# Kernel optimization log

Measured on AMD Instinct MI355X. Metric: run time of the kernel, lower is better.

## Reference

```python
import jax, jax.numpy as jnp
import numpy as np

N_USERS = 200000
N_ITEMS = 200000
F_DIM = 128   # raw embedding_dim of u_feature / i_feature
E_DIM = 64    # embed_dim
N_NODES = 100000
K = 24        # threshold for is_user=True (max sampled neighbors)


def setup_inputs() -> dict:
    key = jax.random.key(0)
    ks = jax.random.split(key, 16)
    s = 0.05
    return {
        "nodes": jax.random.randint(ks[0], (N_NODES,), 0, N_USERS),
        "n_feature": jax.random.normal(ks[1], (N_NODES, E_DIM), jnp.float32),
        "neigh_idx": jax.random.randint(ks[2], (N_NODES, K), 0, N_ITEMS),
        "u_weight": jax.random.normal(ks[3], (N_USERS, F_DIM), jnp.float32) * s,
        "i_weight": jax.random.normal(ks[4], (N_ITEMS, F_DIM), jnp.float32) * s,
        "uW": jax.random.normal(ks[5], (F_DIM, E_DIM), jnp.float32) * s,
        "ub": jax.random.normal(ks[6], (E_DIM,), jnp.float32) * s,
        "iW": jax.random.normal(ks[7], (F_DIM, E_DIM), jnp.float32) * s,
        "ib": jax.random.normal(ks[8], (E_DIM,), jnp.float32) * s,
        "aW1": jax.random.normal(ks[9], (2 * E_DIM, E_DIM), jnp.float32) * s,
        "ab1": jax.random.normal(ks[10], (E_DIM,), jnp.float32) * s,
        "aW2": jax.random.normal(ks[11], (E_DIM, E_DIM), jnp.float32) * s,
        "ab2": jax.random.normal(ks[12], (E_DIM,), jnp.float32) * s,
        "aW3": jax.random.normal(ks[13], (E_DIM, 1), jnp.float32) * s,
        "ab3": jax.random.normal(ks[14], (1,), jnp.float32) * s,
    }


def reference(nodes, n_feature, neigh_idx, u_weight, i_weight,
              uW, ub, iW, ib, aW1, ab1, aW2, ab2, aW3, ab3):
    # u_layer applied to gathered user rows (L0Dense in eval mode ~ dense linear)
    nodes_fea = u_weight[nodes] @ uW + ub                       # [N, d]

    # Project the item table once, then gather neighbors (same math, less traffic
    # than gathering raw features per neighbor): i_layer(ifeature.weight[neighs])
    i_proj = i_weight @ iW + ib                                 # [n_items, d]
    neighs = i_proj[neigh_idx]                                  # [N, K, d]

    # query = mean(node_feature + n_feature[i], dim=0) over a [1,d] tensor == the vector itself
    q = nodes_fea + n_feature                                   # [N, d]

    # attention MLP over concat(neighbor, query) -> softmax over K neighbors
    x = jnp.concatenate(
        [neighs, jnp.broadcast_to(q[:, None, :], neighs.shape)], axis=-1)  # [N, K, 2d]
    h = jax.nn.relu(x @ aW1 + ab1)                              # [N, K, d]
    h = jax.nn.relu(h @ aW2 + ab2)                              # [N, K, d]
    scores = (h @ aW3 + ab3)[..., 0]                            # [N, K]
    att_w = jax.nn.softmax(scores, axis=-1)                     # [N, K]

    # attention-weighted aggregation: neighs_feature.T @ att_w per node
    emb = jnp.einsum('nk,nkd->nd', att_w, neighs)               # [N, d]

    # scatter into the full embed_matrix [num_embeddings, d]
    embed_matrix = jnp.zeros((u_weight.shape[0], nodes_fea.shape[1]),
                             nodes_fea.dtype).at[nodes].set(emb)
    return nodes_fea, embed_matrix
```

## Files before the change

### kernel.cpp

```cpp
#include <hip/hip_runtime.h>
#include <hip/hip_bf16.h>

#define N_NODES 100000
#define N_USERS 200000
#define N_ITEMS 200000
#define KNEI 24
#define E 64
#define F 128

typedef __attribute__((ext_vector_type(8))) short bf16x8;
typedef __attribute__((ext_vector_type(4))) float f32x4;


__device__ inline float bf2f(short s) {
    unsigned u = ((unsigned)(unsigned short)s) << 16;
    return __uint_as_float(u);
}
__device__ inline short f2bf(float f) {
    __hip_bfloat16 h = __float2bfloat16(f);
    return *reinterpret_cast<short*>(&h);
}
__device__ inline float rdlane_f(float v, int l) {
    return __uint_as_float(__builtin_amdgcn_readlane(__float_as_uint(v), l));
}
__device__ inline bf16x8 pack8(float4 a, float4 b) {
    bf16x8 r;
    r[0] = f2bf(a.x); r[1] = f2bf(a.y); r[2] = f2bf(a.z); r[3] = f2bf(a.w);
    r[4] = f2bf(b.x); r[5] = f2bf(b.y); r[6] = f2bf(b.z); r[7] = f2bf(b.w);
    return r;
}

__global__ __launch_bounds__(256) void k_fuse(const float* __restrict__ iW,
                                              const float* __restrict__ aW1,
                                              const float* __restrict__ ib,
                                              const float* __restrict__ ab1,
                                              float* __restrict__ Wp,
                                              float* __restrict__ bp) {
    int g = blockIdx.x * 256 + threadIdx.x;
    int f = g >> 6, c = g & 63;
    float s = 0.f;
    for (int j = 0; j < 64; j++) s = fmaf(iW[f * 64 + j], aW1[j * 64 + c], s);
    Wp[g] = s;
    if (g < 64) {
        float b = ab1[g];
        for (int j = 0; j < 64; j++) b = fmaf(ib[j], aW1[j * 64 + g], b);
        bp[g] = b;
    }
}


__global__ __launch_bounds__(256, 2) void k_item(const float* __restrict__ iwt,
                                                 const float* __restrict__ iW,
                                                 const float* __restrict__ ib,
                                                 const float* __restrict__ Wp,
                                                 const float* __restrict__ bp,
                                                 __hip_bfloat16* __restrict__ iproj,
                                                 __hip_bfloat16* __restrict__ iatt) {
    const int wave = threadIdx.x >> 6, lane = threadIdx.x & 63;
    const int lo = lane & 15, hi = lane >> 4;

    bf16x8 B1[4][4], B2[4][4];
    #pragma unroll
    for (int s = 0; s < 4; s++) {
        #pragma unroll
        for (int u = 0; u < 4; u++) {
            bf16x8 b1, b2;
            #pragma unroll
            for (int e = 0; e < 8; e++) {
                int k = 32 * s + 8 * hi + e;
                b1[e] = f2bf(iW[k * 64 + 16 * u + lo]);
                b2[e] = f2bf(Wp[k * 64 + 16 * u + lo]);
            }
            B1[s][u] = b1; B2[s][u] = b2;
        }
    }
    float bi[4], ba[4];
    #pragma unroll
    for (int u = 0; u < 4; u++) { bi[u] = ib[16 * u + lo]; ba[u] = bp[16 * u + lo]; }

    const int wid = blockIdx.x * 4 + wave;
    for (int t = wid; t < N_ITEMS / 16; t += 512 * 4) {
        int r0 = t * 16;
        const float4* Ap = reinterpret_cast<const float4*>(iwt + (size_t)(r0 + lo) * F);
        bf16x8 A[4];
        #pragma unroll
        for (int s = 0; s < 4; s++)
            A[s] = pack8(Ap[8 * s + 2 * hi], Ap[8 * s + 2 * hi + 1]);
        f32x4 acc1[4], acc2[4];
        #pragma unroll
        for (int u = 0; u < 4; u++) {
            acc1[u] = (f32x4){0.f, 0.f, 0.f, 0.f};
            acc2[u] = (f32x4){0.f, 0.f, 0.f, 0.f};
        }
        #pragma unroll
        for (int s = 0; s < 4; s++) {
            #pragma unroll
            for (int u = 0; u < 4; u++) {
                acc1[u] = __builtin_amdgcn_mfma_f32_16x16x32_bf16(A[s], B1[s][u], acc1[u], 0, 0, 0);
                acc2[u] = __builtin_amdgcn_mfma_f32_16x16x32_bf16(A[s], B2[s][u], acc2[u], 0, 0, 0);
            }
        }
        #pragma unroll
        for (int u = 0; u < 4; u++) {
            #pragma unroll
            for (int reg = 0; reg < 4; reg++) {
                size_t off = (size_t)(r0 + 4 * hi + reg) * E + 16 * u + lo;
                iproj[off] = __float2bfloat16(acc1[u][reg] + bi[u]);
                iatt[off]  = __float2bfloat16(acc2[u][reg] + ba[u]);
            }
        }
    }
}

__global__ __launch_bounds__(256, 2) void k_node1(const int* __restrict__ nodes,
                                                  const float* __restrict__ uwt,
                                                  const float* __restrict__ uW,
                                                  const float* __restrict__ ub,
                                                  float* __restrict__ out_nf,
                                                  int* __restrict__ winner) {
    const int wave = threadIdx.x >> 6, lane = threadIdx.x & 63;
    const int lo = lane & 15, hi = lane >> 4;

    bf16x8 B[4][4];
    #pragma unroll
    for (int s = 0; s < 4; s++) {
        #pragma unroll
        for (int u = 0; u < 4; u++) {
            bf16x8 b;
            #pragma unroll
            for (int e = 0; e < 8; e++) {
                int k = 32 * s + 8 * hi + e;
                b[e] = f2bf(uW[k * 64 + 16 * u + lo]);
            }
            B[s][u] = b;
        }
    }
    float bu[4];
    #pragma unroll
    for (int u = 0; u < 4; u++) bu[u] = ub[16 * u + lo];

    const int wid = blockIdx.x * 4 + wave;
    for (int t = wid; t < N_NODES / 16; t += 256 * 4) {
        int r0 = t * 16;
        int n = r0 + lo;
        int un = nodes[n];
        if (hi == 0) atomicMax(&winner[un], n);
        const float4* Ap = reinterpret_cast<const float4*>(uwt + (size_t)un * F);
        bf16x8 A[4];
        #pragma unroll
        for (int s = 0; s < 4; s++)
            A[s] = pack8(Ap[8 * s + 2 * hi], Ap[8 * s + 2 * hi + 1]);
        f32x4 acc[4];
        #pragma unroll
        for (int u = 0; u < 4; u++) acc[u] = (f32x4){0.f, 0.f, 0.f, 0.f};
        #pragma unroll
        for (int s = 0; s < 4; s++) {
            #pragma unroll
            for (int u = 0; u < 4; u++)
                acc[u] = __builtin_amdgcn_mfma_f32_16x16x32_bf16(A[s], B[s][u], acc[u], 0, 0, 0);
        }
        #pragma unroll
        for (int u = 0; u < 4; u++) {
            #pragma unroll
            for (int reg = 0; reg < 4; reg++)
                out_nf[(size_t)(r0 + 4 * hi + reg) * E + 16 * u + lo] = acc[u][reg] + bu[u];
        }
    }
}

__global__ __launch_bounds__(256, 2) void k_node2(const float* __restrict__ out_nf,
                                                  const float* __restrict__ nfeat,
                                                  const float* __restrict__ aW1,
                                                  __hip_bfloat16* __restrict__ qatt) {
    const int wave = threadIdx.x >> 6, lane = threadIdx.x & 63;
    const int lo = lane & 15, hi = lane >> 4;

    bf16x8 B[2][4];
    #pragma unroll
    for (int s = 0; s < 2; s++) {
        #pragma unroll
        for (int u = 0; u < 4; u++) {
            bf16x8 b;
            #pragma unroll
            for (int e = 0; e < 8; e++) {
                int k = 32 * s + 8 * hi + e;
                b[e] = f2bf(aW1[(size_t)(E + k) * 64 + 16 * u + lo]);
            }
            B[s][u] = b;
        }
    }

    const int wid = blockIdx.x * 4 + wave;
    for (int t = wid; t < N_NODES / 16; t += 256 * 4) {
        int r0 = t * 16;
        const float4* Op = reinterpret_cast<const float4*>(out_nf + (size_t)(r0 + lo) * E);
        const float4* Np = reinterpret_cast<const float4*>(nfeat + (size_t)(r0 + lo) * E);
        bf16x8 A[2];
        #pragma unroll
        for (int s = 0; s < 2; s++) {
            float4 o0 = Op[8 * s + 2 * hi], o1 = Op[8 * s + 2 * hi + 1];
            float4 n0 = Np[8 * s + 2 * hi], n1 = Np[8 * s + 2 * hi + 1];
            float4 q0 = make_float4(o0.x + n0.x, o0.y + n0.y, o0.z + n0.z, o0.w + n0.w);
            float4 q1 = make_float4(o1.x + n1.x, o1.y + n1.y, o1.z + n1.z, o1.w + n1.w);
            A[s] = pack8(q0, q1);
        }
        f32x4 acc[4];
        #pragma unroll
        for (int u = 0; u < 4; u++) acc[u] = (f32x4){0.f, 0.f, 0.f, 0.f};
        #pragma unroll
        for (int s = 0; s < 2; s++) {
            #pragma unroll
            for (int u = 0; u < 4; u++)
                acc[u] = __builtin_amdgcn_mfma_f32_16x16x32_bf16(A[s], B[s][u], acc[u], 0, 0, 0);
        }
        #pragma unroll
        for (int u = 0; u < 4; u++) {
            #pragma unroll
            for (int reg = 0; reg < 4; reg++)
                qatt[(size_t)(r0 + 4 * hi + reg) * E + 16 * u + lo] =
                    __float2bfloat16(acc[u][reg]);
        }
    }
}

__global__ __launch_bounds__(256) void k_att(const int* __restrict__ nodes,
                                             const int* __restrict__ nidx,
                                             const __hip_bfloat16* __restrict__ iproj,
                                             const __hip_bfloat16* __restrict__ iatt,
                                             const __hip_bfloat16* __restrict__ qatt,
                                             const float* __restrict__ aW2,
                                             const float* __restrict__ ab2,
                                             const float* __restrict__ aW3,
                                             const int* __restrict__ winner,
                                             float* __restrict__ outE) {
    __shared__ float s_scores[4][192];
    const int wave = threadIdx.x >> 6, lane = threadIdx.x & 63;
    const int lo = lane & 15, hi = lane >> 4;
    const int n0 = (blockIdx.x * 4 + wave) * 8;

    bf16x8 B[2][4];
    #pragma unroll
    for (int s = 0; s < 2; s++) {
        #pragma unroll
        for (int u = 0; u < 4; u++) {
            bf16x8 b;
            #pragma unroll
            for (int e = 0; e < 8; e++) {
                int kk = 32 * s + 8 * hi + e;
                b[e] = f2bf(aW2[(size_t)kk * E + 16 * u + lo]);
            }
            B[s][u] = b;
        }
    }
    float b2c[4], w3c[4];
    #pragma unroll
    for (int u = 0; u < 4; u++) { b2c[u] = ab2[16 * u + lo]; w3c[u] = aW3[16 * u + lo]; }

    int idxs[12], nls[12];
    #pragma unroll
    for (int t = 0; t < 12; t++) {
        int r = t * 16 + lo;
        int nl = r / 24;
        nls[t] = nl;
        idxs[t] = nidx[(size_t)(n0 + nl) * KNEI + (r - nl * 24)];
    }

    #pragma unroll
    for (int t = 0; t < 12; t++) {
        const bf16x8* iarow = reinterpret_cast<const bf16x8*>(iatt + (size_t)idxs[t] * E);
        const bf16x8* qrow  = reinterpret_cast<const bf16x8*>(qatt + (size_t)(n0 + nls[t]) * E);
        f32x4 acc[4];
        #pragma unroll
        for (int u = 0; u < 4; u++) acc[u] = (f32x4){0.f, 0.f, 0.f, 0.f};
        #pragma unroll
        for (int s = 0; s < 2; s++) {
            bf16x8 ia = iarow[4 * s + hi];
            bf16x8 qa = qrow[4 * s + hi];
            bf16x8 a;
            #pragma unroll
            for (int e = 0; e < 8; e++) {
                float v = bf2f(ia[e]) + bf2f(qa[e]);
                a[e] = f2bf(fmaxf(v, 0.f));
            }
            #pragma unroll
            for (int u = 0; u < 4; u++)
                acc[u] = __builtin_amdgcn_mfma_f32_16x16x32_bf16(a, B[s][u], acc[u], 0, 0, 0);
        }
        f32x4 sum;
        #pragma unroll
        for (int reg = 0; reg < 4; reg++) {
            float v = 0.f;
            #pragma unroll
            for (int u = 0; u < 4; u++)
                v += fmaxf(acc[u][reg] + b2c[u], 0.f) * w3c[u];
            sum[reg] = v;
        }
        #pragma unroll
        for (int m = 1; m < 16; m <<= 1) {
            #pragma unroll
            for (int reg = 0; reg < 4; reg++)
                sum[reg] += __shfl_xor(sum[reg], m);
        }
        if (lo == 0)
            *reinterpret_cast<f32x4*>(&s_scores[wave][t * 16 + hi * 4]) = sum;
    }
    __syncthreads();

    #pragma unroll 1
    for (int nd = 0; nd < 8; nd++) {
        int n = n0 + nd;
        int k5 = lane & 31;
        bool kv = k5 < KNEI;
        float sc = kv ? s_scores[wave][nd * KNEI + k5] : -1e30f;
        float mx = sc;
        #pragma unroll
        for (int m = 1; m < 32; m <<= 1) mx = fmaxf(mx, __shfl_xor(mx, m));
        float e = kv ? __expf(sc - mx) : 0.f;
        float ssum = e;
        #pragma unroll
        for (int m = 1; m < 32; m <<= 1) ssum += __shfl_xor(ssum, m);
        float w = e / ssum;
        int idxv = kv ? nidx[(size_t)n * KNEI + k5] : 0;

        float emb = 0.f;
        const short* ip = reinterpret_cast<const short*>(iproj);
        #pragma unroll
        for (int k = 0; k < KNEI; k++) {
            int sidx = __builtin_amdgcn_readlane(idxv, k);
            float wk = rdlane_f(w, k);
            emb = fmaf(wk, bf2f(ip[(size_t)sidx * E + lane]), emb);
        }
        int un = nodes[n];
        if (winner[un] == n) outE[(size_t)un * E + lane] = emb;
    }
}

extern "C" void kernel_launch(void* const* d_in, const int* in_sizes, int n_in,
                              void* d_out, int out_size, void* d_ws, size_t ws_size,
                              hipStream_t stream) {
    const int*   nodes = (const int*)d_in[0];
    const float* nfeat = (const float*)d_in[1];
    const int*   nidx  = (const int*)d_in[2];
    const float* uwt   = (const float*)d_in[3];
    const float* iwt   = (const float*)d_in[4];
    const float* uW    = (const float*)d_in[5];
    const float* ub    = (const float*)d_in[6];
    const float* iW    = (const float*)d_in[7];
    const float* ib    = (const float*)d_in[8];
    const float* aW1   = (const float*)d_in[9];
    const float* ab1   = (const float*)d_in[10];
    const float* aW2   = (const float*)d_in[11];
    const float* ab2   = (const float*)d_in[12];
    const float* aW3   = (const float*)d_in[13];

    float* out_nf  = (float*)d_out;
    float* out_emb = out_nf + (size_t)N_NODES * E;

    char* ws = (char*)d_ws;
    __hip_bfloat16* iproj = (__hip_bfloat16*)(ws);
    __hip_bfloat16* iatt  = (__hip_bfloat16*)(ws + 25600000);
    __hip_bfloat16* qatt  = (__hip_bfloat16*)(ws + 51200000);
    int*            winner = (int*)(ws + 64000000);
    float*          Wp     = (float*)(ws + 64800000);
    float*          bp     = (float*)(ws + 64832768);

    hipMemsetAsync(winner, 0xFF, (size_t)N_USERS * sizeof(int), stream);
    hipMemsetAsync(out_emb, 0, (size_t)N_USERS * E * sizeof(float), stream);

    k_fuse<<<32, 256, 0, stream>>>(iW, aW1, ib, ab1, Wp, bp);
    k_item<<<512, 256, 0, stream>>>(iwt, iW, ib, Wp, bp, iproj, iatt);
    k_node1<<<256, 256, 0, stream>>>(nodes, uwt, uW, ub, out_nf, winner);
    k_node2<<<256, 256, 0, stream>>>(out_nf, nfeat, aW1, qatt);
    k_att<<<N_NODES / 32, 256, 0, stream>>>(nodes, nidx, iproj, iatt, qatt,
                                            aW2, ab2, aW3, winner, out_emb);
}
```

Measured before the change: 236.8 us.

## Precompute aW2 fragment image and rework attention aggregation to process two nodes per wave

Moves the per-wave bf16 conversion and scattered loading of aW2, ab2 and aW3 into the setup kernel, which writes a lane-ordered fragment image that k_att loads with coalesced 16-byte reads. The ab2 bias is folded into the MFMA accumulator initialisation. The aggregation loop now handles two nodes per wave at once, each half-wave reading 4-byte bf16 pairs of iproj rows, with neighbor index and weight pairs staged in LDS instead of readlane. Outputs are stored as float2. This trades extra LDS traffic and a small amount of setup work for fewer redundant weight loads and wider gathers.

After: 208.1 us. 12.1% less time.

```diff
diff --git a/kernel.cpp b/kernel.cpp
--- a/kernel.cpp
+++ b/kernel.cpp
@@ -20,9 +20,6 @@
     __hip_bfloat16 h = __float2bfloat16(f);
     return *reinterpret_cast<short*>(&h);
 }
-__device__ inline float rdlane_f(float v, int l) {
-    return __uint_as_float(__builtin_amdgcn_readlane(__float_as_uint(v), l));
-}
 __device__ inline bf16x8 pack8(float4 a, float4 b) {
     bf16x8 r;
     r[0] = f2bf(a.x); r[1] = f2bf(a.y); r[2] = f2bf(a.z); r[3] = f2bf(a.w);
@@ -34,17 +31,41 @@
                                               const float* __restrict__ aW1,
                                               const float* __restrict__ ib,
                                               const float* __restrict__ ab1,
+                                              const float* __restrict__ aW2,
+                                              const float* __restrict__ ab2,
+                                              const float* __restrict__ aW3,
                                               float* __restrict__ Wp,
-                                              float* __restrict__ bp) {
+                                              float* __restrict__ bp,
+                                              bf16x8* __restrict__ B2img,
+                                              float* __restrict__ bw) {
     int g = blockIdx.x * 256 + threadIdx.x;
-    int f = g >> 6, c = g & 63;
-    float s = 0.f;
-    for (int j = 0; j < 64; j++) s = fmaf(iW[f * 64 + j], aW1[j * 64 + c], s);
-    Wp[g] = s;
-    if (g < 64) {
-        float b = ab1[g];
-        for (int j = 0; j < 64; j++) b = fmaf(ib[j], aW1[j * 64 + g], b);
-        bp[g] = b;
+    if (g < 8192) {
+        int f = g >> 6, c = g & 63;
+        float s = 0.f;
+        for (int j = 0; j < 64; j++) s = fmaf(iW[f * 64 + j], aW1[j * 64 + c], s);
+        Wp[g] = s;
+        if (g < 64) {
+            float b = ab1[g];
+            for (int j = 0; j < 64; j++) b = fmaf(ib[j], aW1[j * 64 + g], b);
+            bp[g] = b;
+        }
+    } else if (g < 8192 + 512) {
+        int h = g - 8192;
+        int f = h >> 6, l = h & 63;
+        int s = f >> 2, u = f & 3;
+        int lo = l & 15, hi = l >> 4;
+        bf16x8 b;
+        #pragma unroll
+        for (int e = 0; e < 8; e++)
+            b[e] = f2bf(aW2[(size_t)(32 * s + 8 * hi + e) * 64 + 16 * u + lo]);
+        B2img[h] = b;
+        if (f == 0) {
+            #pragma unroll
+            for (int uu = 0; uu < 4; uu++) {
+                bw[l * 8 + uu]     = ab2[16 * uu + lo];
+                bw[l * 8 + 4 + uu] = aW3[16 * uu + lo];
+            }
+        }
     }
 }
 
@@ -228,33 +249,21 @@
                                              const __hip_bfloat16* __restrict__ iproj,
                                              const __hip_bfloat16* __restrict__ iatt,
                                              const __hip_bfloat16* __restrict__ qatt,
-                                             const float* __restrict__ aW2,
-                                             const float* __restrict__ ab2,
-                                             const float* __restrict__ aW3,
+                                             const bf16x8* __restrict__ B2img,
+                                             const float* __restrict__ bw,
                                              const int* __restrict__ winner,
                                              float* __restrict__ outE) {
     __shared__ float s_scores[4][192];
+    __shared__ int2  s_iw[4][192];
     const int wave = threadIdx.x >> 6, lane = threadIdx.x & 63;
     const int lo = lane & 15, hi = lane >> 4;
     const int n0 = (blockIdx.x * 4 + wave) * 8;
 
-    bf16x8 B[2][4];
-    #pragma unroll
-    for (int s = 0; s < 2; s++) {
-        #pragma unroll
-        for (int u = 0; u < 4; u++) {
-            bf16x8 b;
-            #pragma unroll
-            for (int e = 0; e < 8; e++) {
-                int kk = 32 * s + 8 * hi + e;
-                b[e] = f2bf(aW2[(size_t)kk * E + 16 * u + lo]);
-            }
-            B[s][u] = b;
-        }
-    }
-    float b2c[4], w3c[4];
-    #pragma unroll
-    for (int u = 0; u < 4; u++) { b2c[u] = ab2[16 * u + lo]; w3c[u] = aW3[16 * u + lo]; }
+    bf16x8 Bf[8];
+    #pragma unroll
+    for (int f = 0; f < 8; f++) Bf[f] = B2img[f * 64 + lane];
+    f32x4 bb = *reinterpret_cast<const f32x4*>(bw + lane * 8);
+    f32x4 wv = *reinterpret_cast<const f32x4*>(bw + lane * 8 + 4);
 
     int idxs[12], nls[12];
     #pragma unroll
@@ -263,6 +272,7 @@
         int nl = r / 24;
         nls[t] = nl;
         idxs[t] = nidx[(size_t)(n0 + nl) * KNEI + (r - nl * 24)];
+        s_iw[wave][r].x = idxs[t];
     }
 
     #pragma unroll
@@ -271,7 +281,8 @@
         const bf16x8* qrow  = reinterpret_cast<const bf16x8*>(qatt + (size_t)(n0 + nls[t]) * E);
         f32x4 acc[4];
         #pragma unroll
-        for (int u = 0; u < 4; u++) acc[u] = (f32x4){0.f, 0.f, 0.f, 0.f};
+        for (int u = 0; u < 4; u++)
+            acc[u] = (f32x4){bb[u], bb[u], bb[u], bb[u]};
         #pragma unroll
         for (int s = 0; s < 2; s++) {
             bf16x8 ia = iarow[4 * s + hi];
@@ -284,7 +295,7 @@
             }
             #pragma unroll
             for (int u = 0; u < 4; u++)
-                acc[u] = __builtin_amdgcn_mfma_f32_16x16x32_bf16(a, B[s][u], acc[u], 0, 0, 0);
+                acc[u] = __builtin_amdgcn_mfma_f32_16x16x32_bf16(a, Bf[s * 4 + u], acc[u], 0, 0, 0);
         }
         f32x4 sum;
         #pragma unroll
@@ -292,7 +303,7 @@
             float v = 0.f;
             #pragma unroll
             for (int u = 0; u < 4; u++)
-                v += fmaxf(acc[u][reg] + b2c[u], 0.f) * w3c[u];
+                v = fmaf(fmaxf(acc[u][reg], 0.f), wv[u], v);
             sum[reg] = v;
         }
         #pragma unroll
@@ -306,32 +317,37 @@
     }
     __syncthreads();
 
-    #pragma unroll 1
-    for (int nd = 0; nd < 8; nd++) {
+    const int half = lane >> 5, j = lane & 31;
+    for (int p = 0; p < 4; p++) {
+        int nd = 2 * p + half;
         int n = n0 + nd;
-        int k5 = lane & 31;
-        bool kv = k5 < KNEI;
-        float sc = kv ? s_scores[wave][nd * KNEI + k5] : -1e30f;
+        float sc = (j < KNEI) ? s_scores[wave][nd * KNEI + j] : -1e30f;
         float mx = sc;
         #pragma unroll
         for (int m = 1; m < 32; m <<= 1) mx = fmaxf(mx, __shfl_xor(mx, m));
-        float e = kv ? __expf(sc - mx) : 0.f;
-        float ssum = e;
-        #pragma unroll
-        for (int m = 1; m < 32; m <<= 1) ssum += __shfl_xor(ssum, m);
-        float w = e / ssum;
-        int idxv = kv ? nidx[(size_t)n * KNEI + k5] : 0;
-
-        float emb = 0.f;
-        const short* ip = reinterpret_cast<const short*>(iproj);
+        float e = (j < KNEI) ? __expf(sc - mx) : 0.f;
+        float ss = e;
+        #pragma unroll
+        for (int m = 1; m < 32; m <<= 1) ss += __shfl_xor(ss, m);
+        float w = e / ss;
+        if (j < KNEI) s_iw[wave][nd * KNEI + j].y = __float_as_int(w);
+
+        float emb0 = 0.f, emb1 = 0.f;
+        const char* ipb = reinterpret_cast<const char*>(iproj);
         #pragma unroll
         for (int k = 0; k < KNEI; k++) {
-            int sidx = __builtin_amdgcn_readlane(idxv, k);
-            float wk = rdlane_f(w, k);
-            emb = fmaf(wk, bf2f(ip[(size_t)sidx * E + lane]), emb);
+            int2 iw = s_iw[wave][nd * KNEI + k];
+            float wk = __int_as_float(iw.y);
+            unsigned u = *reinterpret_cast<const unsigned*>(
+                ipb + (size_t)iw.x * 128 + j * 4);
+            emb0 = fmaf(wk, __uint_as_float(u << 16), emb0);
+            emb1 = fmaf(wk, __uint_as_float(u & 0xFFFF0000u), emb1);
         }
         int un = nodes[n];
-        if (winner[un] == n) outE[(size_t)un * E + lane] = emb;
+        if (winner[un] == n) {
+            float2 st = make_float2(emb0, emb1);
+            *reinterpret_cast<float2*>(outE + (size_t)un * E + 2 * j) = st;
+        }
     }
 }
 
@@ -363,14 +379,17 @@
     int*            winner = (int*)(ws + 64000000);
     float*          Wp     = (float*)(ws + 64800000);
     float*          bp     = (float*)(ws + 64832768);
+    bf16x8*         B2img  = (bf16x8*)(ws + 64833024);
+    float*          bwimg  = (float*)(ws + 64841216);
 
     hipMemsetAsync(winner, 0xFF, (size_t)N_USERS * sizeof(int), stream);
     hipMemsetAsync(out_emb, 0, (size_t)N_USERS * E * sizeof(float), stream);
 
-    k_fuse<<<32, 256, 0, stream>>>(iW, aW1, ib, ab1, Wp, bp);
+    k_fuse<<<34, 256, 0, stream>>>(iW, aW1, ib, ab1, aW2, ab2, aW3,
+                                   Wp, bp, B2img, bwimg);
     k_item<<<512, 256, 0, stream>>>(iwt, iW, ib, Wp, bp, iproj, iatt);
     k_node1<<<256, 256, 0, stream>>>(nodes, uwt, uW, ub, out_nf, winner);
     k_node2<<<256, 256, 0, stream>>>(out_nf, nfeat, aW1, qatt);
     k_att<<<N_NODES / 32, 256, 0, stream>>>(nodes, nidx, iproj, iatt, qatt,
-                                            aW2, ab2, aW3, winner, out_emb);
-}
+                                            B2img, bwimg, winner, out_emb);
+}
```
